# Optimization experiments

Hardware: AMD Instinct MI355X
Metric: run time of the kernel (lower is better)

Reference implementation:

```python
import jax, jax.numpy as jnp
import numpy as np

EMBED_DIM = 1024
NUM_HEADS = 16
NUM_GLOBAL = 4
NUM_LOCAL = NUM_HEADS - NUM_GLOBAL
WINDOW = 256
HEAD_DIM = EMBED_DIM // NUM_HEADS


def setup_inputs() -> dict:
    key = jax.random.key(0)
    k1, k2, k3 = jax.random.split(key, 3)
    B, S = 4, 2048
    x = jax.random.normal(k1, (B, S, EMBED_DIM), dtype=jnp.float32)
    w_qkv = jax.random.normal(k2, (EMBED_DIM, 3 * EMBED_DIM), dtype=jnp.float32) * (EMBED_DIM ** -0.5)
    b_qkv = jnp.zeros((3 * EMBED_DIM,), dtype=jnp.float32)
    w_out = jax.random.normal(k3, (EMBED_DIM, EMBED_DIM), dtype=jnp.float32) * (EMBED_DIM ** -0.5)
    b_out = jnp.zeros((EMBED_DIM,), dtype=jnp.float32)
    return {"x": x, "w_qkv": w_qkv, "b_qkv": b_qkv, "w_out": w_out, "b_out": b_out}


def _masks(seq_len):
    i = jnp.arange(seq_len)[:, None]
    j = jnp.arange(seq_len)[None, :]
    diff = i - j
    global_mask = diff < 0                      # True = masked (strictly future)
    local_mask = (diff < 0) | (diff > WINDOW)   # True = masked (outside window)
    return global_mask, local_mask


def _attend(q, k, v, mask):
    # q,k,v: [B,h,S,D]; mask: [S,S] True = disallow
    scores = jnp.einsum('bhqd,bhkd->bhqk', q, k) * (HEAD_DIM ** -0.5)
    scores = jnp.where(mask[None, None], -jnp.inf, scores)
    w = jax.nn.softmax(scores, axis=-1)
    return jnp.einsum('bhqk,bhkd->bhqd', w, v)


def reference(x, w_qkv, b_qkv, w_out, b_out):
    B, S, _ = x.shape
    qkv = x @ w_qkv + b_qkv                      # [B,S,3E]
    q, k, v = jnp.split(qkv, 3, axis=-1)
    def heads(t):
        return t.reshape(B, S, NUM_HEADS, HEAD_DIM).transpose(0, 2, 1, 3)
    q, k, v = heads(q), heads(k), heads(v)       # [B,H,S,D]
    gmask, lmask = _masks(S)
    ctx_g = _attend(q[:, :NUM_GLOBAL], k[:, :NUM_GLOBAL], v[:, :NUM_GLOBAL], gmask)
    ctx_l = _attend(q[:, NUM_GLOBAL:], k[:, NUM_GLOBAL:], v[:, NUM_GLOBAL:], lmask)
    ctx = jnp.concatenate([ctx_g, ctx_l], axis=1)          # [B,H,S,D]
    ctx = ctx.transpose(0, 2, 1, 3).reshape(B, S, EMBED_DIM)
    return ctx @ w_out + b_out
```

## Files before the change

kernel.cpp:

```cpp
#include <hip/hip_runtime.h>
#include <stdint.h>

#define EMB 1024
#define SEQ 2048
#define NB 4
#define NH 16
#define HD 64
#define NGLOB 4
#define WIN 256
#define MTOT (NB*SEQ)
#define NQKV (3*EMB)

#define PART_U16 2176

typedef __attribute__((ext_vector_type(8))) short bf16x8;
typedef __attribute__((ext_vector_type(4))) float f32x4;
typedef __attribute__((ext_vector_type(16))) float f32x16;
typedef unsigned short u16;
typedef unsigned int u32;

#define CL2 0.18033688011112042f

#if __has_builtin(__builtin_amdgcn_exp2f)
#define EXP2(x) __builtin_amdgcn_exp2f(x)
#else
#define EXP2(x) exp2f(x)
#endif

__device__ __forceinline__ u16 f2bf(float f) {
  u32 u = __builtin_bit_cast(u32, f);
  u += 0x7fffu + ((u >> 16) & 1u);
  return (u16)(u >> 16);
}

__device__ __forceinline__ float bf2f(u16 v) {
  u32 u = (u32)v << 16;
  return __builtin_bit_cast(float, u);
}

__device__ __forceinline__ u32 packtrunc(float a, float b) {
  u32 ua = __builtin_bit_cast(u32, a);
  u32 ub = __builtin_bit_cast(u32, b);
  return (ua >> 16) | (ub & 0xffff0000u);
}

#define MFMA16(a, b, c) __builtin_amdgcn_mfma_f32_16x16x32_bf16(a, b, c, 0, 0, 0)
#define MFMA32(a, b, c) __builtin_amdgcn_mfma_f32_32x32x16_bf16(a, b, c, 0, 0, 0)
#define GLD16(g, l) __builtin_amdgcn_global_load_lds( \
    (const __attribute__((address_space(1))) void*)(g), \
    (__attribute__((address_space(3))) void*)(l), 16, 0, 0)

__global__ void k_cast(const float* __restrict__ in, u16* __restrict__ out, int n4) {
  int i = blockIdx.x * blockDim.x + threadIdx.x;
  if (i >= n4) return;
  float4 f = ((const float4*)in)[i];
  ushort4 o;
  o.x = f2bf(f.x); o.y = f2bf(f.y); o.z = f2bf(f.z); o.w = f2bf(f.w);
  ((ushort4*)out)[i] = o;
}

__global__ void k_transpose_cast(const float* __restrict__ w, u16* __restrict__ wt,
                                 int R, int C) {
  __shared__ float tile[32][33];
  int c0 = blockIdx.x * 32, r0 = blockIdx.y * 32;
  int tx = threadIdx.x, ty = threadIdx.y;
  #pragma unroll
  for (int j = 0; j < 32; j += 8)
    tile[ty + j][tx] = w[(size_t)(r0 + ty + j) * C + (c0 + tx)];
  __syncthreads();
  #pragma unroll
  for (int j = 0; j < 32; j += 8)
    wt[(size_t)(c0 + ty + j) * R + (r0 + tx)] = f2bf(tile[tx][ty + j]);
}

template <int EPI>
__global__ __launch_bounds__(256, 2) void k_gemm(
    const u16* __restrict__ A, const u16* __restrict__ Bt,
    const float* __restrict__ bias,
    u16* __restrict__ Qo, u16* __restrict__ Ko, u16* __restrict__ Vt,
    float* __restrict__ outp) {
  __shared__ __align__(16) u16 ldsA[128 * 64];
  __shared__ __align__(16) u16 ldsB[128 * 64];
  const int tid = threadIdx.x;
  const int w = tid >> 6, lane = tid & 63;
  const int wm = w >> 1, wn = w & 1;
  const int m0 = blockIdx.x * 128, n0 = blockIdx.y * 128;
  const int rq = lane & 15, g = lane >> 4;

  const int srow = lane >> 3;
  const int scol = ((lane & 7) ^ srow) << 3;

  f32x4 acc[4][4] = {};
  char* ldsAb = (char*)ldsA;
  char* ldsBb = (char*)ldsB;

  for (int k0 = 0; k0 < EMB; k0 += 64) {
    #pragma unroll
    for (int it = 0; it < 4; ++it) {
      int t = w * 4 + it;
      int row = t * 8 + srow;
      GLD16(A + (size_t)(m0 + row) * EMB + k0 + scol, ldsAb + t * 1024);
      GLD16(Bt + (size_t)(n0 + row) * EMB + k0 + scol, ldsBb + t * 1024);
    }
    __syncthreads();
    #pragma unroll
    for (int ks = 0; ks < 2; ++ks) {
      bf16x8 af[4], bfr[4];
      #pragma unroll
      for (int i = 0; i < 4; ++i) {
        int rowA = wm * 64 + i * 16 + rq;
        int off = (ks * 64 + (g << 4)) ^ ((rowA & 7) << 4);
        af[i] = *(const bf16x8*)(ldsAb + rowA * 128 + off);
        int rowB = wn * 64 + i * 16 + rq;
        int offb = (ks * 64 + (g << 4)) ^ ((rowB & 7) << 4);
        bfr[i] = *(const bf16x8*)(ldsBb + rowB * 128 + offb);
      }
      #pragma unroll
      for (int mi = 0; mi < 4; ++mi)
        #pragma unroll
        for (int ni = 0; ni < 4; ++ni)
          acc[mi][ni] = MFMA16(af[mi], bfr[ni], acc[mi][ni]);
    }
    __syncthreads();
  }

  #pragma unroll
  for (int ni = 0; ni < 4; ++ni) {
    int col = n0 + wn * 64 + ni * 16 + rq;
    float bv = bias[col];
    if (EPI == 0) {
      int part = col >> 10;
      int hh = (col & 1023) >> 6;
      int d = col & 63;
      #pragma unroll
      for (int mi = 0; mi < 4; ++mi) {
        #pragma unroll
        for (int i = 0; i < 4; ++i) {
          int m = m0 + wm * 64 + mi * 16 + g * 4 + i;
          int b = m >> 11, s = m & 2047;
          u16 val = f2bf(acc[mi][ni][i] + bv);
          size_t bh = (size_t)(b * NH + hh);
          if (part == 0)      Qo[(bh * SEQ + s) * HD + d] = val;
          else if (part == 1) Ko[(bh * SEQ + s) * HD + d] = val;
          else                Vt[((bh * 128 + (s >> 4)) * 64 + d) * 16 + (s & 15)] = val;
        }
      }
    } else {
      #pragma unroll
      for (int mi = 0; mi < 4; ++mi)
        #pragma unroll
        for (int i = 0; i < 4; ++i) {
          int m = m0 + wm * 64 + mi * 16 + g * 4 + i;
          outp[(size_t)m * EMB + col] = acc[mi][ni][i] + bv;
        }
    }
  }
}

__global__ __launch_bounds__(256, 4) void k_attn(
    const u16* __restrict__ Q, const u16* __restrict__ K,
    const u16* __restrict__ Vt, u16* __restrict__ ctx,
    u16* __restrict__ part) {
  const int w = threadIdx.x >> 6, lane = threadIdx.x & 63;
  const int l31 = lane & 31;
  const int hi = lane >> 5;
  const bool hib = hi != 0;
  const int hi8 = hi * 8, hi4 = hi * 4;

  const int gid = blockIdx.x;
  const bool isglob = gid < 1024;

  int bh, qt, cstart, clen;
  if (isglob) {
    int bg = gid & 15;
    int j = gid >> 4;
    qt = ((j & 3) << 4) | (j >> 2);
    bh = (bg >> 2) * 16 + (bg & 3);
    int L = qt + 1;
    int base = L >> 2, rem = L & 3;
    clen = base + (w < rem ? 1 : 0);
    cstart = w * base + (w < rem ? w : rem);
  } else {
    int lidx = (gid - 1024) * 4 + w;
    int bl = lidx >> 6;
    bh = (bl / 12) * 16 + 4 + (bl % 12);
    qt = lidx & 63;
    int qb_ = qt * 32;
    int klo = (qb_ > WIN) ? qb_ - WIN : 0;
    cstart = klo >> 5;
    clen = qt + 1 - cstart;
  }

  const int qb = qt * 32;
  const int h = bh & 15;
  const int b = bh >> 4;
  const bool isloc = !isglob;

  const u16* Qp = Q + (size_t)bh * SEQ * HD;
  const u16* Kp = K + (size_t)bh * SEQ * HD;
  const u16* Vp = Vt + (size_t)bh * SEQ * HD;

  const int q = qb + l31;
  const float NINF = -__builtin_inff();

  bf16x8 qf[4];
  #pragma unroll
  for (int j = 0; j < 4; ++j)
    qf[j] = *(const bf16x8*)(Qp + (size_t)q * HD + j * 16 + hi8);

  f32x16 oacc[2] = {};
  float m = NINF;
  float l = 0.f;

  int kc = cstart * 32;
  #pragma unroll 2
  for (int it = 0; it < clen; ++it, kc += 32) {
    bf16x8 kf0, kf1, kf2, kf3, vf[2][2];
    {
      const u16* Kr = Kp + (size_t)(kc + l31) * HD + hi8;
      kf0 = *(const bf16x8*)(Kr);
      kf1 = *(const bf16x8*)(Kr + 16);
      kf2 = *(const bf16x8*)(Kr + 32);
      kf3 = *(const bf16x8*)(Kr + 48);
      const u16* Vb = Vp + (size_t)(kc >> 4) * 1024 + hi8;
      #pragma unroll
      for (int dt = 0; dt < 2; ++dt)
        #pragma unroll
        for (int sl = 0; sl < 2; ++sl)
          vf[dt][sl] = *(const bf16x8*)(Vb + (sl * 64 + dt * 32 + l31) * 16);
    }

    f32x16 s0 = {}, s1 = {};
    s0 = MFMA32(kf0, qf[0], s0);
    s1 = MFMA32(kf2, qf[2], s1);
    s0 = MFMA32(kf1, qf[1], s0);
    s1 = MFMA32(kf3, qf[3], s1);

    const bool needs_mask = (kc == qb) || (isloc && (qb - kc > 225));
    float p[16];
    float cmax = NINF;
    if (needs_mask) {
      #pragma unroll
      for (int r = 0; r < 16; ++r) {
        int key = kc + hi4 + (r & 3) + 8 * (r >> 2);
        float v = s0[r] + s1[r];
        bool bad = (key > q) || (isloc && (q - key > WIN));
        p[r] = bad ? NINF : v;
        cmax = fmaxf(cmax, p[r]);
      }
    } else {
      #pragma unroll
      for (int r = 0; r < 16; ++r) {
        p[r] = s0[r] + s1[r];
        cmax = fmaxf(cmax, p[r]);
      }
    }
    cmax = fmaxf(cmax, __shfl_xor(cmax, 32));

    float muC;
    if (__any(cmax > m + 64.f)) {
      float mn = fmaxf(m, cmax);
      muC = (mn == NINF) ? 0.f : mn * CL2;
      float oldC = (m == NINF) ? muC : m * CL2;
      float f = EXP2(oldC - muC);
      m = mn;
      l *= f;
      #pragma unroll
      for (int dt = 0; dt < 2; ++dt)
        #pragma unroll
        for (int r = 0; r < 16; ++r)
          oacc[dt][r] *= f;
    } else {
      muC = (m == NINF) ? 0.f : m * CL2;
    }

    float psum = 0.f;
    #pragma unroll
    for (int r = 0; r < 16; ++r) {
      float e = EXP2(__builtin_fmaf(p[r], CL2, -muC));
      p[r] = e;
      psum += e;
    }
    psum += __shfl_xor(psum, 32);
    l += psum;

    union { u32 u[4]; bf16x8 v; } pbf[2];
    #pragma unroll
    for (int sl = 0; sl < 2; ++sl) {
      int s8 = sl * 8;
      u32 X0 = packtrunc(p[s8 + 0], p[s8 + 1]);
      u32 X1 = packtrunc(p[s8 + 2], p[s8 + 3]);
      u32 X2 = packtrunc(p[s8 + 4], p[s8 + 5]);
      u32 X3 = packtrunc(p[s8 + 6], p[s8 + 7]);
      u32 oX0 = (u32)__shfl_xor((int)X0, 32);
      u32 oX1 = (u32)__shfl_xor((int)X1, 32);
      u32 oX2 = (u32)__shfl_xor((int)X2, 32);
      u32 oX3 = (u32)__shfl_xor((int)X3, 32);
      pbf[sl].u[0] = hib ? oX2 : X0;
      pbf[sl].u[1] = hib ? oX3 : X1;
      pbf[sl].u[2] = hib ? X2 : oX0;
      pbf[sl].u[3] = hib ? X3 : oX1;
    }

    #pragma unroll
    for (int dt = 0; dt < 2; ++dt)
      #pragma unroll
      for (int sl = 0; sl < 2; ++sl)
        oacc[dt] = MFMA32(vf[dt][sl], pbf[sl].v, oacc[dt]);
  }

  if (isglob) {
    u16* PB = part + (size_t)(gid * 4 + w) * PART_U16;
    #pragma unroll
    for (int dt = 0; dt < 2; ++dt)
      #pragma unroll
      for (int r = 0; r < 16; ++r) {
        int d = dt * 32 + hi4 + (r & 3) + 8 * (r >> 2);
        PB[d * 32 + l31] = f2bf(oacc[dt][r]);
      }
    float* PF = (float*)(PB + 2048);
    if (hi == 0) { PF[l31] = m; PF[32 + l31] = l; }
  } else {
    float linv = 1.f / l;
    #pragma unroll
    for (int dt = 0; dt < 2; ++dt) {
      #pragma unroll
      for (int r = 0; r < 16; ++r) {
        int d = dt * 32 + hi4 + (r & 3) + 8 * (r >> 2);
        int e = h * HD + d;
        ctx[(size_t)(b * SEQ + q) * EMB + e] = f2bf(oacc[dt][r] * linv);
      }
    }
  }
}

__global__ __launch_bounds__(256, 4) void k_merge(
    const u16* __restrict__ part, u16* __restrict__ ctx) {
  const int t = blockIdx.x;
  const int bg = t & 15;
  const int j = t >> 4;
  const int qt = ((j & 3) << 4) | (j >> 2);
  const int bh = (bg >> 2) * 16 + (bg & 3);
  const int qb = qt * 32;
  const int h = bh & 15;
  const int b = bh >> 4;

  const u16* P0 = part + (size_t)(t * 4 + 0) * PART_U16;
  const u16* P1 = part + (size_t)(t * 4 + 1) * PART_U16;
  const u16* P2 = part + (size_t)(t * 4 + 2) * PART_U16;
  const u16* P3 = part + (size_t)(t * 4 + 3) * PART_U16;
  const float* F0 = (const float*)(P0 + 2048);
  const float* F1 = (const float*)(P1 + 2048);
  const float* F2 = (const float*)(P2 + 2048);
  const float* F3 = (const float*)(P3 + 2048);

  const int tid = threadIdx.x;
  const int dd = tid & 63;
  const int qg = tid >> 6;
  #pragma unroll
  for (int i = 0; i < 8; ++i) {
    int qq = qg * 8 + i;
    float m0v = F0[qq], m1v = F1[qq], m2v = F2[qq], m3v = F3[qq];
    float M = fmaxf(fmaxf(m0v, m1v), fmaxf(m2v, m3v));
    float w0 = __expf((m0v - M) * 0.125f), w1 = __expf((m1v - M) * 0.125f);
    float w2 = __expf((m2v - M) * 0.125f), w3 = __expf((m3v - M) * 0.125f);
    float L = w0 * F0[32 + qq] + w1 * F1[32 + qq] +
              w2 * F2[32 + qq] + w3 * F3[32 + qq];
    float val = w0 * bf2f(P0[dd * 32 + qq]) + w1 * bf2f(P1[dd * 32 + qq]) +
                w2 * bf2f(P2[dd * 32 + qq]) + w3 * bf2f(P3[dd * 32 + qq]);
    int s = qb + qq;
    ctx[(size_t)(b * SEQ + s) * EMB + h * HD + dd] = f2bf(val / L);
  }
}

extern "C" void kernel_launch(void* const* d_in, const int* in_sizes, int n_in,
                              void* d_out, int out_size, void* d_ws, size_t ws_size,
                              hipStream_t stream) {
  const float* x     = (const float*)d_in[0];
  const float* w_qkv = (const float*)d_in[1];
  const float* b_qkv = (const float*)d_in[2];
  const float* w_out = (const float*)d_in[3];
  const float* b_out = (const float*)d_in[4];
  float* out = (float*)d_out;

  char* ws = (char*)d_ws;
  u16* xb    = (u16*)(ws);
  u16* wqkvT = (u16*)(ws + (16ull << 20));
  u16* woutT = (u16*)(ws + (22ull << 20));
  u16* Qb    = (u16*)(ws + (24ull << 20));
  u16* Kb    = (u16*)(ws + (40ull << 20));
  u16* Vt    = (u16*)(ws + (56ull << 20));
  u16* ctx   = (u16*)(ws + (72ull << 20));
  u16* part  = xb;

  k_cast<<<(MTOT * EMB / 4) / 256, 256, 0, stream>>>(x, xb, MTOT * EMB / 4);
  dim3 tb(32, 8);
  k_transpose_cast<<<dim3(NQKV / 32, EMB / 32), tb, 0, stream>>>(w_qkv, wqkvT, EMB, NQKV);
  k_transpose_cast<<<dim3(EMB / 32, EMB / 32), tb, 0, stream>>>(w_out, woutT, EMB, EMB);

  k_gemm<0><<<dim3(MTOT / 128, NQKV / 128), 256, 0, stream>>>(
      xb, wqkvT, b_qkv, Qb, Kb, Vt, nullptr);

  k_attn<<<dim3(1024 + 768), 256, 0, stream>>>(Qb, Kb, Vt, ctx, part);
  k_merge<<<dim3(1024), 256, 0, stream>>>(part, ctx);

  k_gemm<1><<<dim3(MTOT / 128, EMB / 128), 256, 0, stream>>>(
      ctx, woutT, b_out, nullptr, nullptr, nullptr, out);
}
```

Before: 197.6 us.

## Split global-head attention into variable key segments proportional to query tile position

Global causal heads previously always split each query tile's key range across 4 waves, regardless of length. Now the number of segments grows with the query tile index (1 to 8 segments in bands of 9 tiles), so each wave handles a roughly equal number of key chunks. The merge kernel loops over the variable segment count. This balances wave work and reduces per-wave tail latency, at the cost of more partial buffers, more merge traffic, and more complex index math.

Result: slower. 213.6 us (+8.1%).

```diff
diff --git a/kernel.cpp b/kernel.cpp
--- a/kernel.cpp
+++ b/kernel.cpp
@@ -12,6 +12,8 @@
 #define NQKV (3*EMB)
 
 #define PART_U16 2176
+#define NGJOBS 4160
+#define NLJOBS 3072
 
 typedef __attribute__((ext_vector_type(8))) short bf16x8;
 typedef __attribute__((ext_vector_type(4))) float f32x4;
@@ -43,6 +45,7 @@
   u32 ub = __builtin_bit_cast(u32, b);
   return (ua >> 16) | (ub & 0xffff0000u);
 }
+
 
 #define MFMA16(a, b, c) __builtin_amdgcn_mfma_f32_16x16x32_bf16(a, b, c, 0, 0, 0)
 #define MFMA32(a, b, c) __builtin_amdgcn_mfma_f32_32x32x16_bf16(a, b, c, 0, 0, 0)
@@ -167,21 +170,25 @@
   const bool hib = hi != 0;
   const int hi8 = hi * 8, hi4 = hi * 4;
 
-  const int gid = blockIdx.x;
-  const bool isglob = gid < 1024;
+  const int j = blockIdx.x * 4 + w;
+  const bool isglob = j < NGJOBS;
 
   int bh, qt, cstart, clen;
   if (isglob) {
-    int bg = gid & 15;
-    int j = gid >> 4;
-    qt = ((j & 3) << 4) | (j >> 2);
+    int rem = j, b = 0;
+    while (b < 7 && rem >= 144 * (b + 1)) { rem -= 144 * (b + 1); ++b; }
+    int nseg = b + 1;
+    int qoff = (rem >> 4) / nseg;
+    int r2 = rem - qoff * 16 * nseg;
+    int seg = r2 >> 4, bg = r2 & 15;
+    qt = 9 * b + qoff;
     bh = (bg >> 2) * 16 + (bg & 3);
     int L = qt + 1;
-    int base = L >> 2, rem = L & 3;
-    clen = base + (w < rem ? 1 : 0);
-    cstart = w * base + (w < rem ? w : rem);
+    int base = L / nseg, rm = L - base * nseg;
+    clen = base + (seg < rm ? 1 : 0);
+    cstart = seg * base + (seg < rm ? seg : rm);
   } else {
-    int lidx = (gid - 1024) * 4 + w;
+    int lidx = j - NGJOBS;
     int bl = lidx >> 6;
     bh = (bl / 12) * 16 + 4 + (bl % 12);
     qt = lidx & 63;
@@ -193,7 +200,7 @@
 
   const int qb = qt * 32;
   const int h = bh & 15;
-  const int b = bh >> 4;
+  const int b_ = bh >> 4;
   const bool isloc = !isglob;
 
   const u16* Qp = Q + (size_t)bh * SEQ * HD;
@@ -205,8 +212,8 @@
 
   bf16x8 qf[4];
   #pragma unroll
-  for (int j = 0; j < 4; ++j)
-    qf[j] = *(const bf16x8*)(Qp + (size_t)q * HD + j * 16 + hi8);
+  for (int jj = 0; jj < 4; ++jj)
+    qf[jj] = *(const bf16x8*)(Qp + (size_t)q * HD + jj * 16 + hi8);
 
   f32x16 oacc[2] = {};
   float m = NINF;
@@ -310,7 +317,7 @@
   }
 
   if (isglob) {
-    u16* PB = part + (size_t)(gid * 4 + w) * PART_U16;
+    u16* PB = part + (size_t)j * PART_U16;
     #pragma unroll
     for (int dt = 0; dt < 2; ++dt)
       #pragma unroll
@@ -328,7 +335,7 @@
       for (int r = 0; r < 16; ++r) {
         int d = dt * 32 + hi4 + (r & 3) + 8 * (r >> 2);
         int e = h * HD + d;
-        ctx[(size_t)(b * SEQ + q) * EMB + e] = f2bf(oacc[dt][r] * linv);
+        ctx[(size_t)(b_ * SEQ + q) * EMB + e] = f2bf(oacc[dt][r] * linv);
       }
     }
   }
@@ -338,21 +345,14 @@
     const u16* __restrict__ part, u16* __restrict__ ctx) {
   const int t = blockIdx.x;
   const int bg = t & 15;
-  const int j = t >> 4;
-  const int qt = ((j & 3) << 4) | (j >> 2);
+  const int qt = t >> 4;
+  const int b = qt / 9;
+  const int nseg = b + 1;
+  const int jbase = 72 * b * (b + 1) + (qt - 9 * b) * 16 * nseg + bg;
   const int bh = (bg >> 2) * 16 + (bg & 3);
   const int qb = qt * 32;
   const int h = bh & 15;
-  const int b = bh >> 4;
-
-  const u16* P0 = part + (size_t)(t * 4 + 0) * PART_U16;
-  const u16* P1 = part + (size_t)(t * 4 + 1) * PART_U16;
-  const u16* P2 = part + (size_t)(t * 4 + 2) * PART_U16;
-  const u16* P3 = part + (size_t)(t * 4 + 3) * PART_U16;
-  const float* F0 = (const float*)(P0 + 2048);
-  const float* F1 = (const float*)(P1 + 2048);
-  const float* F2 = (const float*)(P2 + 2048);
-  const float* F3 = (const float*)(P3 + 2048);
+  const int bb = bh >> 4;
 
   const int tid = threadIdx.x;
   const int dd = tid & 63;
@@ -360,16 +360,21 @@
   #pragma unroll
   for (int i = 0; i < 8; ++i) {
     int qq = qg * 8 + i;
-    float m0v = F0[qq], m1v = F1[qq], m2v = F2[qq], m3v = F3[qq];
-    float M = fmaxf(fmaxf(m0v, m1v), fmaxf(m2v, m3v));
-    float w0 = __expf((m0v - M) * 0.125f), w1 = __expf((m1v - M) * 0.125f);
-    float w2 = __expf((m2v - M) * 0.125f), w3 = __expf((m3v - M) * 0.125f);
-    float L = w0 * F0[32 + qq] + w1 * F1[32 + qq] +
-              w2 * F2[32 + qq] + w3 * F3[32 + qq];
-    float val = w0 * bf2f(P0[dd * 32 + qq]) + w1 * bf2f(P1[dd * 32 + qq]) +
-                w2 * bf2f(P2[dd * 32 + qq]) + w3 * bf2f(P3[dd * 32 + qq]);
-    int s = qb + qq;
-    ctx[(size_t)(b * SEQ + s) * EMB + h * HD + dd] = f2bf(val / L);
+    float M = -__builtin_inff();
+    for (int s = 0; s < nseg; ++s) {
+      const float* F = (const float*)(part + (size_t)(jbase + s * 16) * PART_U16 + 2048);
+      M = fmaxf(M, F[qq]);
+    }
+    float L = 0.f, val = 0.f;
+    for (int s = 0; s < nseg; ++s) {
+      const u16* P = part + (size_t)(jbase + s * 16) * PART_U16;
+      const float* F = (const float*)(P + 2048);
+      float wgt = EXP2((F[qq] - M) * CL2);
+      L += wgt * F[32 + qq];
+      val += wgt * bf2f(P[dd * 32 + qq]);
+    }
+    int s_ = qb + qq;
+    ctx[(size_t)(bb * SEQ + s_) * EMB + h * HD + dd] = f2bf(val / L);
   }
 }
 
@@ -401,7 +406,7 @@
   k_gemm<0><<<dim3(MTOT / 128, NQKV / 128), 256, 0, stream>>>(
       xb, wqkvT, b_qkv, Qb, Kb, Vt, nullptr);
 
-  k_attn<<<dim3(1024 + 768), 256, 0, stream>>>(Qb, Kb, Vt, ctx, part);
+  k_attn<<<dim3((NGJOBS + NLJOBS) / 4), 256, 0, stream>>>(Qb, Kb, Vt, ctx, part);
   k_merge<<<dim3(1024), 256, 0, stream>>>(part, ctx);
 
   k_gemm<1><<<dim3(MTOT / 128, EMB / 128), 256, 0, stream>>>(
```
